# Kernel optimization log

Hardware: AMD Instinct MI355X
Metric: run time of the kernel (lower is better)

The kernel has to match this reference:

```python
import jax, jax.numpy as jnp
import numpy as np

HID = 1024
H = 8
HD = HID // H  # 128; KV length must equal HD for the bias-add broadcast
B = 8
LQ = 4096
LK = HD


def setup_inputs() -> dict:
    key = jax.random.key(0)
    ks = jax.random.split(key, 16)
    s = 0.02
    inp = {
        "query": jax.random.normal(ks[0], (B, LQ, HID), jnp.float32),
        "key": jax.random.normal(ks[1], (B, LK, HID), jnp.float32),
        "value": jax.random.normal(ks[2], (B, LK, HID), jnp.float32),
        "atten": jax.random.normal(ks[3], (B, LQ, HID), jnp.float32),
        "mask": jax.random.randint(ks[4], (B, 1, 1, LK), 0, 2, jnp.int32),
        "Wq": jax.random.normal(ks[5], (HID, HID), jnp.float32) * s,
        "bq": jnp.zeros((HID,), jnp.float32),
        "Wk": jax.random.normal(ks[6], (HID, HID), jnp.float32) * s,
        "bk": jnp.zeros((HID,), jnp.float32),
        "Wv": jax.random.normal(ks[7], (HID, HID), jnp.float32) * s,
        "bv": jnp.zeros((HID,), jnp.float32),
        "Watt": jax.random.normal(ks[8], (HID, HID), jnp.float32) * s,
        "batt": jnp.zeros((HID,), jnp.float32),
        "Wfc": jax.random.normal(ks[9], (HID, HID), jnp.float32) * s,
        "bfc": jnp.zeros((HID,), jnp.float32),
    }
    return inp


def _heads(x):
    # [B, L, HID] -> [B, H, L, HD]
    b, l, _ = x.shape
    return x.reshape(b, l, H, HD).transpose(0, 2, 1, 3)


def reference(query, key, value, atten, mask, Wq, bq, Wk, bk, Wv, bv, Watt, batt, Wfc, bfc):
    scale = jnp.sqrt(jnp.asarray(HD, jnp.float32))
    atten_out = _heads(atten @ Watt.T + batt)          # [B,H,LQ,HD]
    Q = _heads(query @ Wq.T + bq)                      # [B,H,LQ,HD]
    K = _heads(key @ Wk.T + bk)                        # [B,H,LK,HD]
    V = _heads(value @ Wv.T + bv)                      # [B,H,LK,HD]
    energy = jnp.einsum('bhqd,bhkd->bhqk', Q, K) / scale + atten_out  # LK == HD
    energy = jnp.where(mask == 0, jnp.float32(-1e10), energy)
    attention = jax.nn.softmax(energy, axis=-1)
    x = jnp.einsum('bhqk,bhkd->bhqd', attention, V)
    x = x.transpose(0, 2, 1, 3).reshape(query.shape[0], -1, HID)
    return x @ Wfc.T + bfc
```

## Files before the change

### kernel.cpp

```cpp
#include <hip/hip_runtime.h>
#include <hip/hip_bf16.h>
#include <stdint.h>

typedef __bf16 bf16_t;
typedef __bf16 bf16x8 __attribute__((ext_vector_type(8)));
typedef __bf16 bf16x4 __attribute__((ext_vector_type(4)));
typedef float f32x4 __attribute__((ext_vector_type(4)));

#define HIDN 1024
#define NHEAD 8
#define HDIM 128
#define NBATCH 8
#define LQLEN 4096
#define LKLEN 128

__device__ __forceinline__ void gload_lds16(const void* g, void* l) {
  __builtin_amdgcn_global_load_lds(
      (const __attribute__((address_space(1))) unsigned int*)g,
      (__attribute__((address_space(3))) unsigned int*)l, 16, 0, 0);
}

__global__ __launch_bounds__(256) void convk(const float* __restrict__ in,
                                             bf16_t* __restrict__ out, int n4) {
  int i = blockIdx.x * blockDim.x + threadIdx.x;
  const int stride = gridDim.x * blockDim.x;
  for (; i < n4; i += stride) {
    const float4 v = ((const float4*)in)[i];
    bf16x4 o;
    o[0] = (bf16_t)v.x; o[1] = (bf16_t)v.y; o[2] = (bf16_t)v.z; o[3] = (bf16_t)v.w;
    ((bf16x4*)out)[i] = o;
  }
}

template <int MODE>
__global__ __launch_bounds__(512, 2) void gemm8p(const bf16_t* __restrict__ A,
                                                 const bf16_t* __restrict__ Bw,
                                                 const float* __restrict__ bias,
                                                 void* __restrict__ Cout) {
  constexpr int NT = 32;
  constexpr int SLOT = 32768;
  __shared__ uint4 smem_raw[8192];
  char* smem = (char*)smem_raw;

  const int tid = threadIdx.x;
  const int wid = tid >> 6, lane = tid & 63;
  const int lr = lane & 15, lh = lane >> 4;
  const int wr = wid >> 2, wc = wid & 3;

  const int bid = blockIdx.x;
  const int m_blk = (bid & 7) * 16 + (bid >> 5);
  const int n_blk = (bid >> 3) & 3;
  const int m0 = m_blk * 256, n0 = n_blk * 256;

  const int c0 = tid, c1 = tid + 512;
  const int sc0 = (((c0 & 3) ^ ((c0 >> 3) & 3)) << 4);
  const int sc1 = (((c1 & 3) ^ ((c1 >> 3) & 3)) << 4);
  const char* srcA0 = (const char*)A + (size_t)(m0 + (c0 >> 2)) * 2048 + sc0;
  const char* srcA1 = (const char*)A + (size_t)(m0 + (c1 >> 2)) * 2048 + sc1;
  const char* srcB0 = (const char*)Bw + (size_t)(n0 + (c0 >> 2)) * 2048 + sc0;
  const char* srcB1 = (const char*)Bw + (size_t)(n0 + (c1 >> 2)) * 2048 + sc1;
  const int d0 = c0 * 16, d1 = c1 * 16;

  f32x4 acc[8][4] = {};

#pragma unroll
  for (int tt = 0; tt < 3; ++tt) {
    char* dst = smem + tt * SLOT;
    gload_lds16(srcA0 + tt * 64, dst + d0);
    gload_lds16(srcA1 + tt * 64, dst + d1);
    gload_lds16(srcB0 + tt * 64, dst + 16384 + d0);
    gload_lds16(srcB1 + tt * 64, dst + 16384 + d1);
  }
  asm volatile("s_waitcnt vmcnt(8)" ::: "memory");
  __builtin_amdgcn_s_barrier();
  __builtin_amdgcn_sched_barrier(0);

  const int swz = ((lr >> 1) & 3) << 4;
  const int aoff = (wr * 128 + lr) * 64 + ((lh << 4) ^ swz);
  const int boff = 16384 + (wc * 64 + lr) * 64 + ((lh << 4) ^ swz);

  for (int t = 0; t < NT; ++t) {
    const char* sA = smem + (t & 3) * SLOT + aoff;
    const char* sB = smem + (t & 3) * SLOT + boff;
    char* dst = smem + ((t + 3) & 3) * SLOT;
    const int kb = (t + 3) * 64;
    const bool pf = (t <= NT - 4);

    bf16x8 bfr[4], af[8];
#pragma unroll
    for (int n = 0; n < 4; ++n) bfr[n] = *(const bf16x8*)(sB + n * 1024);
#pragma unroll
    for (int m = 0; m < 8; ++m) af[m] = *(const bf16x8*)(sA + m * 1024);
    if (pf) {
      gload_lds16(srcA0 + kb, dst + d0);
      gload_lds16(srcA1 + kb, dst + d1);
      gload_lds16(srcB0 + kb, dst + 16384 + d0);
      gload_lds16(srcB1 + kb, dst + 16384 + d1);
    }
    __builtin_amdgcn_s_setprio(1);
#pragma unroll
    for (int m = 0; m < 8; ++m)
#pragma unroll
      for (int n = 0; n < 4; ++n)
        acc[m][n] = __builtin_amdgcn_mfma_f32_16x16x32_bf16(af[m], bfr[n], acc[m][n], 0, 0, 0);
    __builtin_amdgcn_s_setprio(0);

    if (t < NT - 1) {
      __builtin_amdgcn_sched_barrier(0);
      if (t <= NT - 4)
        asm volatile("s_waitcnt vmcnt(8)" ::: "memory");
      else if (t == NT - 3)
        asm volatile("s_waitcnt vmcnt(4)" ::: "memory");
      else
        asm volatile("s_waitcnt vmcnt(0)" ::: "memory");
      __builtin_amdgcn_s_barrier();
      __builtin_amdgcn_sched_barrier(0);
    }
  }

  if constexpr (MODE == 2) {
    float* C = (float*)Cout;
#pragma unroll
    for (int f = 0; f < 8; ++f) {
      const int gm = m0 + wr * 128 + f * 16 + lh * 4;
#pragma unroll
      for (int j = 0; j < 4; ++j) {
        const int gn = n0 + wc * 64 + j * 16 + lr;
        const float bb = bias[gn];
#pragma unroll
        for (int r = 0; r < 4; ++r)
          C[(size_t)(gm + r) * HIDN + gn] = acc[f][j][r] + bb;
      }
    }
  } else {
    __builtin_amdgcn_s_barrier();
    __builtin_amdgcn_sched_barrier(0);
    char* wlds = smem + wid * 16384;
#pragma unroll
    for (int f = 0; f < 8; ++f) {
#pragma unroll
      for (int j = 0; j < 4; ++j) {
        const int gn = n0 + wc * 64 + j * 16 + lr;
        const float bb = bias[gn];
#pragma unroll
        for (int r = 0; r < 4; ++r)
          *(bf16_t*)(wlds + (f * 16 + lh * 4 + r) * 128 + (j * 16 + lr) * 2) =
              (bf16_t)(acc[f][j][r] + bb);
      }
    }
    asm volatile("s_waitcnt lgkmcnt(0)" ::: "memory");
    __builtin_amdgcn_sched_barrier(0);
    bf16_t* C = (bf16_t*)Cout;
    const int gnb = n0 + wc * 64;
    const int h = gnb >> 7, dd = gnb & 127;
#pragma unroll
    for (int p = 0; p < 16; ++p) {
      const int rl = p * 8 + (lane >> 3);
      const int cb = (lane & 7) * 16;
      const uint4 v = *(const uint4*)(wlds + rl * 128 + cb);
      const int gm = m0 + wr * 128 + rl;
      const int b = gm >> 12, l = gm & 4095;
      char* dstp = (char*)(C + (((size_t)(b * NHEAD + h) * LQLEN + l) << 7) + dd) + cb;
      *(uint4*)dstp = v;
    }
  }
}

template <int MODE, int LROW>
__global__ __launch_bounds__(256) void gemm_bt(const bf16_t* __restrict__ A,
                                               const bf16_t* __restrict__ Bw,
                                               const float* __restrict__ bias,
                                               void* __restrict__ Cout) {
  constexpr int BK = 32;
  __shared__ uint4 AsRaw[128 * BK * 2 / 16];
  __shared__ uint4 BsRaw[128 * BK * 2 / 16];
  bf16_t* As = (bf16_t*)AsRaw;
  bf16_t* Bs = (bf16_t*)BsRaw;

  const int tid = threadIdx.x;
  const int wid = tid >> 6;
  const int lane = tid & 63;
  const int lr = lane & 15, lh = lane >> 4;
  const int m0 = blockIdx.x * 128, n0 = blockIdx.y * 128;
  const int wm = (wid >> 1) * 64, wn = (wid & 1) * 64;

  f32x4 acc[4][4] = {};

  const int srow = lane >> 2;
  const int scol = (lane & 3) * 16;

  for (int k0 = 0; k0 < HIDN; k0 += BK) {
#pragma unroll
    for (int i = 0; i < 2; ++i) {
      const int c = wid + i * 4;
      const int row = c * 16 + srow;
      gload_lds16((const char*)A + ((size_t)(m0 + row) * HIDN + k0) * 2 + scol,
                  (char*)As + c * 1024);
      gload_lds16((const char*)Bw + ((size_t)(n0 + row) * HIDN + k0) * 2 + scol,
                  (char*)Bs + c * 1024);
    }
    __syncthreads();

    bf16x8 af[4], bfr[4];
#pragma unroll
    for (int i = 0; i < 4; ++i) {
      af[i]  = *(const bf16x8*)(As + (wm + i * 16 + lr) * BK + lh * 8);
      bfr[i] = *(const bf16x8*)(Bs + (wn + i * 16 + lr) * BK + lh * 8);
    }
#pragma unroll
    for (int i = 0; i < 4; ++i)
#pragma unroll
      for (int j = 0; j < 4; ++j)
        acc[i][j] = __builtin_amdgcn_mfma_f32_16x16x32_bf16(af[i], bfr[j], acc[i][j], 0, 0, 0);
    __syncthreads();
  }

#pragma unroll
  for (int i = 0; i < 4; ++i) {
#pragma unroll
    for (int r = 0; r < 4; ++r) {
      const int gm = m0 + wm + i * 16 + lh * 4 + r;
#pragma unroll
      for (int j = 0; j < 4; ++j) {
        const int gn = n0 + wn + j * 16 + lr;
        const float v = acc[i][j][r] + bias[gn];
        const int b = gm / LROW, l = gm - b * LROW;
        const int h = gn >> 7, d = gn & 127;
        size_t idx;
        if constexpr (MODE == 0)
          idx = (((size_t)(b * NHEAD + h) * LROW + l) << 7) + d;
        else
          idx = (((size_t)(b * NHEAD + h) * 128 + d) << 7) + l;
        ((bf16_t*)Cout)[idx] = (bf16_t)v;
      }
    }
  }
}

__global__ __launch_bounds__(256) void attn_kernel(
    const bf16_t* __restrict__ Qh, const bf16_t* __restrict__ Ah,
    const bf16_t* __restrict__ Kh, const bf16_t* __restrict__ Vt,
    const int* __restrict__ mask, bf16_t* __restrict__ X) {
  __shared__ uint4 KsRaw[2048];
  __shared__ uint4 VsRaw[2048];
  __shared__ float Ms[128];
  char* Ks = (char*)KsRaw;
  char* Vs = (char*)VsRaw;

  const int tid = threadIdx.x, wid = tid >> 6, lane = tid & 63;
  const int lr = lane & 15, lh = lane >> 4;
  const int bh = blockIdx.y, b = bh >> 3, h = bh & 7;
  const int q0 = blockIdx.x * 64;

  {
    const char* Kg = (const char*)(Kh + (size_t)bh * 16384);
    const char* Vg = (const char*)(Vt + (size_t)bh * 16384);
#pragma unroll
    for (int it = 0; it < 8; ++it) {
      const int e = it * 256 + tid;
      const int row = e >> 4;
      const int cb = (e & 15) << 4;
      const int dst = row * 256 + (cb ^ ((row & 7) << 4));
      *(uint4*)(Ks + dst) = *(const uint4*)(Kg + row * 256 + cb);
      *(uint4*)(Vs + dst) = *(const uint4*)(Vg + row * 256 + cb);
    }
  }
  if (tid < 128) Ms[tid] = (mask[b * 128 + tid] == 0) ? 0.f : 1.f;

  bf16x8 qf[4];
  {
    const bf16_t* Qb = Qh + ((size_t)bh * LQLEN + q0 + wid * 16 + lr) * 128;
#pragma unroll
    for (int s = 0; s < 4; ++s) qf[s] = *(const bf16x8*)(Qb + s * 32 + lh * 8);
  }
  __syncthreads();

  f32x4 acc[8] = {};
#pragma unroll
  for (int nt = 0; nt < 8; ++nt) {
#pragma unroll
    for (int s = 0; s < 4; ++s) {
      const int row = nt * 16 + lr;
      const int cb = (s * 64 + lh * 16) ^ ((row & 7) << 4);
      const bf16x8 kf = *(const bf16x8*)(Ks + row * 256 + cb);
      acc[nt] = __builtin_amdgcn_mfma_f32_16x16x32_bf16(qf[s], kf, acc[nt], 0, 0, 0);
    }
  }

  float ex[8][4];
  float rsum[4];
  const float sc = 0.08838834764831845f;
  const bf16_t* Ab = Ah + ((size_t)bh * LQLEN + q0 + wid * 16) * 128;
#pragma unroll
  for (int r = 0; r < 4; ++r) {
    const int row = lh * 4 + r;
    float mx = -3.0e38f;
#pragma unroll
    for (int nt = 0; nt < 8; ++nt) {
      const int col = nt * 16 + lr;
      float e = acc[nt][r] * sc + (float)Ab[row * 128 + col];
      e = (Ms[col] != 0.f) ? e : -1.0e10f;
      ex[nt][r] = e;
      mx = fmaxf(mx, e);
    }
    mx = fmaxf(mx, __shfl_xor(mx, 1));
    mx = fmaxf(mx, __shfl_xor(mx, 2));
    mx = fmaxf(mx, __shfl_xor(mx, 4));
    mx = fmaxf(mx, __shfl_xor(mx, 8));
    float s_ = 0.f;
#pragma unroll
    for (int nt = 0; nt < 8; ++nt) {
      const float p = expf(ex[nt][r] - mx);
      ex[nt][r] = p;
      s_ += p;
    }
    s_ += __shfl_xor(s_, 1);
    s_ += __shfl_xor(s_, 2);
    s_ += __shfl_xor(s_, 4);
    s_ += __shfl_xor(s_, 8);
    rsum[r] = s_;
  }

  __syncthreads();
  char* Pb = Ks + wid * 4096;
#pragma unroll
  for (int r = 0; r < 4; ++r) {
    const int row = lh * 4 + r;
#pragma unroll
    for (int nt = 0; nt < 8; ++nt) {
      const int col = nt * 16 + lr;
      const int off = (row * 256 + col * 2) ^ ((row & 7) << 4);
      *(bf16_t*)(Pb + off) = (bf16_t)ex[nt][r];
    }
  }
  __syncthreads();

  bf16x8 pf[4];
#pragma unroll
  for (int s = 0; s < 4; ++s)
    pf[s] = *(const bf16x8*)(Pb + lr * 256 + ((s * 64 + lh * 16) ^ ((lr & 7) << 4)));
  f32x4 acc2[8] = {};
#pragma unroll
  for (int nt = 0; nt < 8; ++nt) {
#pragma unroll
    for (int s = 0; s < 4; ++s) {
      const int row = nt * 16 + lr;
      const int cb = (s * 64 + lh * 16) ^ ((row & 7) << 4);
      const bf16x8 vf = *(const bf16x8*)(Vs + row * 256 + cb);
      acc2[nt] = __builtin_amdgcn_mfma_f32_16x16x32_bf16(pf[s], vf, acc2[nt], 0, 0, 0);
    }
  }

  float rs[4];
#pragma unroll
  for (int r = 0; r < 4; ++r) rs[r] = 1.f / rsum[r];
  bf16_t* Xb = X + ((size_t)b * LQLEN + q0 + wid * 16) * HIDN + h * 128;
#pragma unroll
  for (int nt = 0; nt < 8; ++nt)
#pragma unroll
    for (int r = 0; r < 4; ++r)
      Xb[(size_t)(lh * 4 + r) * HIDN + nt * 16 + lr] = (bf16_t)(acc2[nt][r] * rs[r]);
}

extern "C" void kernel_launch(void* const* d_in, const int* in_sizes, int n_in,
                              void* d_out, int out_size, void* d_ws, size_t ws_size,
                              hipStream_t stream) {
  const float* query = (const float*)d_in[0];
  const float* key   = (const float*)d_in[1];
  const float* value = (const float*)d_in[2];
  const float* atten = (const float*)d_in[3];
  const int*   mask  = (const int*)d_in[4];
  const float* Wq  = (const float*)d_in[5];  const float* bq   = (const float*)d_in[6];
  const float* Wk  = (const float*)d_in[7];  const float* bk   = (const float*)d_in[8];
  const float* Wv  = (const float*)d_in[9];  const float* bv   = (const float*)d_in[10];
  const float* Wat = (const float*)d_in[11]; const float* batt = (const float*)d_in[12];
  const float* Wfc = (const float*)d_in[13]; const float* bfc  = (const float*)d_in[14];

  char* ws = (char*)d_ws;
  bf16_t* qbf = (bf16_t*)(ws + 0x0000000);
  bf16_t* abf = (bf16_t*)(ws + 0x4000000);
  bf16_t* Qh  = (bf16_t*)(ws + 0x8000000);
  bf16_t* Ah  = (bf16_t*)(ws + 0xC000000);
  char* sm = ws + 0x10000000;
  bf16_t* kbf = (bf16_t*)(sm + 0x000000);
  bf16_t* vbf = (bf16_t*)(sm + 0x200000);
  bf16_t* wqb = (bf16_t*)(sm + 0x400000);
  bf16_t* wkb = (bf16_t*)(sm + 0x600000);
  bf16_t* wvb = (bf16_t*)(sm + 0x800000);
  bf16_t* wab = (bf16_t*)(sm + 0xA00000);
  bf16_t* wfb = (bf16_t*)(sm + 0xC00000);
  bf16_t* Kh  = (bf16_t*)(sm + 0xE00000);
  bf16_t* Vt  = (bf16_t*)(sm + 0x1000000);
  bf16_t* X   = qbf;

  auto conv = [&](const float* src, bf16_t* dst, int n) {
    const int n4 = n >> 2;
    int g = (n4 + 255) >> 8; if (g > 2048) g = 2048;
    convk<<<dim3(g), dim3(256), 0, stream>>>(src, dst, n4);
  };
  conv(query, qbf, NBATCH * LQLEN * HIDN);
  conv(atten, abf, NBATCH * LQLEN * HIDN);
  conv(key,   kbf, NBATCH * LKLEN * HIDN);
  conv(value, vbf, NBATCH * LKLEN * HIDN);
  conv(Wq,  wqb, HIDN * HIDN);
  conv(Wk,  wkb, HIDN * HIDN);
  conv(Wv,  wvb, HIDN * HIDN);
  conv(Wat, wab, HIDN * HIDN);
  conv(Wfc, wfb, HIDN * HIDN);

  gemm_bt<0, 128><<<dim3(8, 8), dim3(256), 0, stream>>>(kbf, wkb, bk, (void*)Kh);
  gemm_bt<1, 128><<<dim3(8, 8), dim3(256), 0, stream>>>(vbf, wvb, bv, (void*)Vt);

  gemm8p<0><<<dim3(512), dim3(512), 0, stream>>>(qbf, wqb, bq, (void*)Qh);
  gemm8p<0><<<dim3(512), dim3(512), 0, stream>>>(abf, wab, batt, (void*)Ah);

  attn_kernel<<<dim3(LQLEN / 64, NBATCH * NHEAD), dim3(256), 0, stream>>>(
      Qh, Ah, Kh, Vt, mask, X);

  gemm8p<2><<<dim3(512), dim3(512), 0, stream>>>(X, wfb, bfc, d_out);
}
```

Measured before the change: 466.8 us.

## Fuse fp32-to-bf16 conversion of activations into GEMM loads; batch weight conversions

The Q and attention projection GEMMs now read fp32 activations directly through registers, convert them to bf16 and write them to LDS inside a software-pipelined loop. This removes the separate full-size conversion passes over query and atten. The seven small conversions are merged into one launch. The attention kernel also stages the Ah tile in LDS with async loads and writes its output through LDS as coalesced 16-byte stores. In exchange, the A path now uses register staging rather than direct-to-LDS loads, which raises register pressure and makes the waitcnt bookkeeping more delicate.

```diff
diff --git a/kernel.cpp b/kernel.cpp
--- a/kernel.cpp
+++ b/kernel.cpp
@@ -4,7 +4,6 @@
 
 typedef __bf16 bf16_t;
 typedef __bf16 bf16x8 __attribute__((ext_vector_type(8)));
-typedef __bf16 bf16x4 __attribute__((ext_vector_type(4)));
 typedef float f32x4 __attribute__((ext_vector_type(4)));
 
 #define HIDN 1024
@@ -20,20 +19,33 @@
       (__attribute__((address_space(3))) unsigned int*)l, 16, 0, 0);
 }
 
-__global__ __launch_bounds__(256) void convk(const float* __restrict__ in,
-                                             bf16_t* __restrict__ out, int n4) {
-  int i = blockIdx.x * blockDim.x + threadIdx.x;
-  const int stride = gridDim.x * blockDim.x;
-  for (; i < n4; i += stride) {
-    const float4 v = ((const float4*)in)[i];
-    bf16x4 o;
+__global__ __launch_bounds__(256) void convk7(
+    const float* s0, const float* s1, const float* s2, const float* s3,
+    const float* s4, const float* s5, const float* s6,
+    bf16_t* d0, bf16_t* d1, bf16_t* d2, bf16_t* d3,
+    bf16_t* d4, bf16_t* d5, bf16_t* d6) {
+  const float* src; bf16_t* dst;
+  switch (blockIdx.y) {
+    case 0: src = s0; dst = d0; break;
+    case 1: src = s1; dst = d1; break;
+    case 2: src = s2; dst = d2; break;
+    case 3: src = s3; dst = d3; break;
+    case 4: src = s4; dst = d4; break;
+    case 5: src = s5; dst = d5; break;
+    default: src = s6; dst = d6; break;
+  }
+  const int n4 = (1024 * 1024) / 4;
+  const int stride = gridDim.x * 256;
+  for (int i = blockIdx.x * 256 + threadIdx.x; i < n4; i += stride) {
+    const float4 v = ((const float4*)src)[i];
+    bf16x8 o;
     o[0] = (bf16_t)v.x; o[1] = (bf16_t)v.y; o[2] = (bf16_t)v.z; o[3] = (bf16_t)v.w;
-    ((bf16x4*)out)[i] = o;
+    *(uint2*)((char*)dst + (size_t)i * 8) = *(uint2*)&o;
   }
 }
 
-template <int MODE>
-__global__ __launch_bounds__(512, 2) void gemm8p(const bf16_t* __restrict__ A,
+template <int MODE, bool AF32>
+__global__ __launch_bounds__(512, 2) void gemm8p(const void* __restrict__ Asrc,
                                                  const bf16_t* __restrict__ Bw,
                                                  const float* __restrict__ bias,
                                                  void* __restrict__ Cout) {
@@ -53,70 +65,162 @@
   const int m0 = m_blk * 256, n0 = n_blk * 256;
 
   const int c0 = tid, c1 = tid + 512;
-  const int sc0 = (((c0 & 3) ^ ((c0 >> 3) & 3)) << 4);
-  const int sc1 = (((c1 & 3) ^ ((c1 >> 3) & 3)) << 4);
-  const char* srcA0 = (const char*)A + (size_t)(m0 + (c0 >> 2)) * 2048 + sc0;
-  const char* srcA1 = (const char*)A + (size_t)(m0 + (c1 >> 2)) * 2048 + sc1;
-  const char* srcB0 = (const char*)Bw + (size_t)(n0 + (c0 >> 2)) * 2048 + sc0;
-  const char* srcB1 = (const char*)Bw + (size_t)(n0 + (c1 >> 2)) * 2048 + sc1;
+  const int sl0 = ((c0 & 3) ^ ((c0 >> 3) & 3));
+  const int sl1 = ((c1 & 3) ^ ((c1 >> 3) & 3));
+  const char* srcB0 = (const char*)Bw + (size_t)(n0 + (c0 >> 2)) * 2048 + (sl0 << 4);
+  const char* srcB1 = (const char*)Bw + (size_t)(n0 + (c1 >> 2)) * 2048 + (sl1 << 4);
   const int d0 = c0 * 16, d1 = c1 * 16;
 
   f32x4 acc[8][4] = {};
-
-#pragma unroll
-  for (int tt = 0; tt < 3; ++tt) {
-    char* dst = smem + tt * SLOT;
-    gload_lds16(srcA0 + tt * 64, dst + d0);
-    gload_lds16(srcA1 + tt * 64, dst + d1);
-    gload_lds16(srcB0 + tt * 64, dst + 16384 + d0);
-    gload_lds16(srcB1 + tt * 64, dst + 16384 + d1);
-  }
-  asm volatile("s_waitcnt vmcnt(8)" ::: "memory");
-  __builtin_amdgcn_s_barrier();
-  __builtin_amdgcn_sched_barrier(0);
 
   const int swz = ((lr >> 1) & 3) << 4;
   const int aoff = (wr * 128 + lr) * 64 + ((lh << 4) ^ swz);
   const int boff = 16384 + (wc * 64 + lr) * 64 + ((lh << 4) ^ swz);
 
-  for (int t = 0; t < NT; ++t) {
-    const char* sA = smem + (t & 3) * SLOT + aoff;
-    const char* sB = smem + (t & 3) * SLOT + boff;
-    char* dst = smem + ((t + 3) & 3) * SLOT;
-    const int kb = (t + 3) * 64;
-    const bool pf = (t <= NT - 4);
-
-    bf16x8 bfr[4], af[8];
-#pragma unroll
-    for (int n = 0; n < 4; ++n) bfr[n] = *(const bf16x8*)(sB + n * 1024);
-#pragma unroll
-    for (int m = 0; m < 8; ++m) af[m] = *(const bf16x8*)(sA + m * 1024);
-    if (pf) {
-      gload_lds16(srcA0 + kb, dst + d0);
-      gload_lds16(srcA1 + kb, dst + d1);
-      gload_lds16(srcB0 + kb, dst + 16384 + d0);
-      gload_lds16(srcB1 + kb, dst + 16384 + d1);
-    }
-    __builtin_amdgcn_s_setprio(1);
-#pragma unroll
-    for (int m = 0; m < 8; ++m)
-#pragma unroll
-      for (int n = 0; n < 4; ++n)
-        acc[m][n] = __builtin_amdgcn_mfma_f32_16x16x32_bf16(af[m], bfr[n], acc[m][n], 0, 0, 0);
-    __builtin_amdgcn_s_setprio(0);
-
-    if (t < NT - 1) {
-      __builtin_amdgcn_sched_barrier(0);
-      if (t <= NT - 4)
-        asm volatile("s_waitcnt vmcnt(8)" ::: "memory");
-      else if (t == NT - 3)
-        asm volatile("s_waitcnt vmcnt(4)" ::: "memory");
-      else
-        asm volatile("s_waitcnt vmcnt(0)" ::: "memory");
-      __builtin_amdgcn_s_barrier();
-      __builtin_amdgcn_sched_barrier(0);
-    }
-  }
+#define GLOADB(T)                                                     \
+  do {                                                                \
+    char* bdst = smem + (((T) & 3) * SLOT) + 16384;                   \
+    gload_lds16(srcB0 + (T) * 64, bdst + d0);                         \
+    gload_lds16(srcB1 + (T) * 64, bdst + d1);                         \
+  } while (0)
+
+  if constexpr (AF32) {
+    const char* srcAf0 = (const char*)Asrc + (size_t)(m0 + (c0 >> 2)) * 4096 + sl0 * 32;
+    const char* srcAf1 = (const char*)Asrc + (size_t)(m0 + (c1 >> 2)) * 4096 + sl1 * 32;
+
+    f32x4 eA0, eA1, eA2, eA3, oA0, oA1, oA2, oA3;
+
+#define ISSUE_A(R0, R1, R2, R3, T)                                    \
+  do {                                                                \
+    R0 = *(const f32x4*)(srcAf0 + (T) * 128);                         \
+    R1 = *(const f32x4*)(srcAf0 + (T) * 128 + 16);                    \
+    R2 = *(const f32x4*)(srcAf1 + (T) * 128);                         \
+    R3 = *(const f32x4*)(srcAf1 + (T) * 128 + 16);                    \
+  } while (0)
+
+#define WRITE_A(SL, R0, R1, R2, R3)                                   \
+  do {                                                                \
+    bf16x8 w0, w1;                                                    \
+    w0[0] = (bf16_t)R0[0]; w0[1] = (bf16_t)R0[1];                     \
+    w0[2] = (bf16_t)R0[2]; w0[3] = (bf16_t)R0[3];                     \
+    w0[4] = (bf16_t)R1[0]; w0[5] = (bf16_t)R1[1];                     \
+    w0[6] = (bf16_t)R1[2]; w0[7] = (bf16_t)R1[3];                     \
+    w1[0] = (bf16_t)R2[0]; w1[1] = (bf16_t)R2[1];                     \
+    w1[2] = (bf16_t)R2[2]; w1[3] = (bf16_t)R2[3];                     \
+    w1[4] = (bf16_t)R3[0]; w1[5] = (bf16_t)R3[1];                     \
+    w1[6] = (bf16_t)R3[2]; w1[7] = (bf16_t)R3[3];                     \
+    *(bf16x8*)(smem + (SL) * SLOT + d0) = w0;                         \
+    *(bf16x8*)(smem + (SL) * SLOT + d1) = w1;                         \
+  } while (0)
+
+    ISSUE_A(eA0, eA1, eA2, eA3, 0);
+    ISSUE_A(oA0, oA1, oA2, oA3, 1);
+    asm volatile("" ::: "memory");
+    GLOADB(0); GLOADB(1); GLOADB(2);
+    asm volatile("" ::: "memory");
+    asm volatile("s_waitcnt vmcnt(6)" ::: "memory");
+    WRITE_A(0, eA0, eA1, eA2, eA3);
+    WRITE_A(1, oA0, oA1, oA2, oA3);
+    ISSUE_A(eA0, eA1, eA2, eA3, 2);
+    ISSUE_A(oA0, oA1, oA2, oA3, 3);
+    asm volatile("" ::: "memory");
+    asm volatile("s_waitcnt vmcnt(4) lgkmcnt(0)" ::: "memory");
+    __builtin_amdgcn_s_barrier();
+    __builtin_amdgcn_sched_barrier(0);
+
+#define GTILE(T, R0, R1, R2, R3)                                          \
+  do {                                                                    \
+    const char* sA = smem + ((T) & 3) * SLOT + aoff;                      \
+    const char* sB = smem + ((T) & 3) * SLOT + boff;                      \
+    if ((T) <= NT - 3) WRITE_A(((T) + 2) & 3, R0, R1, R2, R3);            \
+    if ((T) <= NT - 5) ISSUE_A(R0, R1, R2, R3, (T) + 4);                  \
+    if ((T) <= NT - 4) GLOADB((T) + 3);                                   \
+    bf16x8 bfr[4], af[8];                                                 \
+    _Pragma("unroll") for (int n = 0; n < 4; ++n)                         \
+        bfr[n] = *(const bf16x8*)(sB + n * 1024);                         \
+    _Pragma("unroll") for (int m = 0; m < 8; ++m)                         \
+        af[m] = *(const bf16x8*)(sA + m * 1024);                          \
+    __builtin_amdgcn_s_setprio(1);                                        \
+    _Pragma("unroll") for (int m = 0; m < 8; ++m)                         \
+        _Pragma("unroll") for (int n = 0; n < 4; ++n)                     \
+            acc[m][n] = __builtin_amdgcn_mfma_f32_16x16x32_bf16(          \
+                af[m], bfr[n], acc[m][n], 0, 0, 0);                       \
+    __builtin_amdgcn_s_setprio(0);                                        \
+    if ((T) < NT - 1) {                                                   \
+      __builtin_amdgcn_sched_barrier(0);                                  \
+      if ((T) <= NT - 5)                                                  \
+        asm volatile("s_waitcnt vmcnt(6) lgkmcnt(0)" ::: "memory");       \
+      else if ((T) <= NT - 3)                                             \
+        asm volatile("s_waitcnt vmcnt(2) lgkmcnt(0)" ::: "memory");       \
+      else                                                                \
+        asm volatile("s_waitcnt vmcnt(0) lgkmcnt(0)" ::: "memory");       \
+      __builtin_amdgcn_s_barrier();                                       \
+      __builtin_amdgcn_sched_barrier(0);                                  \
+    }                                                                     \
+  } while (0)
+
+    for (int tt = 0; tt < NT / 2; ++tt) {
+      GTILE(2 * tt, eA0, eA1, eA2, eA3);
+      GTILE(2 * tt + 1, oA0, oA1, oA2, oA3);
+    }
+#undef GTILE
+#undef ISSUE_A
+#undef WRITE_A
+  } else {
+    const char* srcA0 = (const char*)Asrc + (size_t)(m0 + (c0 >> 2)) * 2048 + (sl0 << 4);
+    const char* srcA1 = (const char*)Asrc + (size_t)(m0 + (c1 >> 2)) * 2048 + (sl1 << 4);
+#pragma unroll
+    for (int tt = 0; tt < 3; ++tt) {
+      char* dst = smem + tt * SLOT;
+      gload_lds16(srcA0 + tt * 64, dst + d0);
+      gload_lds16(srcA1 + tt * 64, dst + d1);
+      gload_lds16(srcB0 + tt * 64, dst + 16384 + d0);
+      gload_lds16(srcB1 + tt * 64, dst + 16384 + d1);
+    }
+    asm volatile("s_waitcnt vmcnt(8)" ::: "memory");
+    __builtin_amdgcn_s_barrier();
+    __builtin_amdgcn_sched_barrier(0);
+
+    for (int t = 0; t < NT; ++t) {
+      const char* sA = smem + (t & 3) * SLOT + aoff;
+      const char* sB = smem + (t & 3) * SLOT + boff;
+      char* dst = smem + ((t + 3) & 3) * SLOT;
+      const int kb = (t + 3) * 64;
+      const bool pf = (t <= NT - 4);
+
+      bf16x8 bfr[4], af[8];
+#pragma unroll
+      for (int n = 0; n < 4; ++n) bfr[n] = *(const bf16x8*)(sB + n * 1024);
+#pragma unroll
+      for (int m = 0; m < 8; ++m) af[m] = *(const bf16x8*)(sA + m * 1024);
+      if (pf) {
+        gload_lds16(srcA0 + kb, dst + d0);
+        gload_lds16(srcA1 + kb, dst + d1);
+        gload_lds16(srcB0 + kb, dst + 16384 + d0);
+        gload_lds16(srcB1 + kb, dst + 16384 + d1);
+      }
+      __builtin_amdgcn_s_setprio(1);
+#pragma unroll
+      for (int m = 0; m < 8; ++m)
+#pragma unroll
+        for (int n = 0; n < 4; ++n)
+          acc[m][n] = __builtin_amdgcn_mfma_f32_16x16x32_bf16(af[m], bfr[n], acc[m][n], 0, 0, 0);
+      __builtin_amdgcn_s_setprio(0);
+
+      if (t < NT - 1) {
+        __builtin_amdgcn_sched_barrier(0);
+        if (t <= NT - 4)
+          asm volatile("s_waitcnt vmcnt(8)" ::: "memory");
+        else if (t == NT - 3)
+          asm volatile("s_waitcnt vmcnt(4)" ::: "memory");
+        else
+          asm volatile("s_waitcnt vmcnt(0)" ::: "memory");
+        __builtin_amdgcn_s_barrier();
+        __builtin_amdgcn_sched_barrier(0);
+      }
+    }
+  }
+#undef GLOADB
 
   if constexpr (MODE == 2) {
     float* C = (float*)Cout;
@@ -286,19 +390,32 @@
       acc[nt] = __builtin_amdgcn_mfma_f32_16x16x32_bf16(qf[s], kf, acc[nt], 0, 0, 0);
     }
   }
+  __syncthreads();
+
+  {
+    const char* Ag = (const char*)(Ah + ((size_t)bh * LQLEN + q0) * 128);
+#pragma unroll
+    for (int it = 0; it < 4; ++it) {
+      const int c = it * 256 + tid;
+      gload_lds16(Ag + c * 16, Ks + 16384 + c * 16);
+    }
+  }
+  asm volatile("s_waitcnt vmcnt(0)" ::: "memory");
+  __syncthreads();
+  const char* Al = Ks + 16384;
 
   float ex[8][4];
   float rsum[4];
   const float sc = 0.08838834764831845f;
-  const bf16_t* Ab = Ah + ((size_t)bh * LQLEN + q0 + wid * 16) * 128;
 #pragma unroll
   for (int r = 0; r < 4; ++r) {
     const int row = lh * 4 + r;
+    const int rowg = wid * 16 + row;
     float mx = -3.0e38f;
 #pragma unroll
     for (int nt = 0; nt < 8; ++nt) {
       const int col = nt * 16 + lr;
-      float e = acc[nt][r] * sc + (float)Ab[row * 128 + col];
+      float e = acc[nt][r] * sc + (float)(*(const bf16_t*)(Al + rowg * 256 + col * 2));
       e = (Ms[col] != 0.f) ? e : -1.0e10f;
       ex[nt][r] = e;
       mx = fmaxf(mx, e);
@@ -321,7 +438,6 @@
     rsum[r] = s_;
   }
 
-  __syncthreads();
   char* Pb = Ks + wid * 4096;
 #pragma unroll
   for (int r = 0; r < 4; ++r) {
@@ -350,16 +466,29 @@
       acc2[nt] = __builtin_amdgcn_mfma_f32_16x16x32_bf16(pf[s], vf, acc2[nt], 0, 0, 0);
     }
   }
+  __syncthreads();
 
   float rs[4];
 #pragma unroll
   for (int r = 0; r < 4; ++r) rs[r] = 1.f / rsum[r];
-  bf16_t* Xb = X + ((size_t)b * LQLEN + q0 + wid * 16) * HIDN + h * 128;
 #pragma unroll
   for (int nt = 0; nt < 8; ++nt)
 #pragma unroll
     for (int r = 0; r < 4; ++r)
-      Xb[(size_t)(lh * 4 + r) * HIDN + nt * 16 + lr] = (bf16_t)(acc2[nt][r] * rs[r]);
+      *(bf16_t*)(Vs + (wid * 16 + lh * 4 + r) * 256 + (nt * 16 + lr) * 2) =
+          (bf16_t)(acc2[nt][r] * rs[r]);
+  asm volatile("s_waitcnt lgkmcnt(0)" ::: "memory");
+  __syncthreads();
+
+#pragma unroll
+  for (int it = 0; it < 4; ++it) {
+    const int c = it * 256 + tid;
+    const int row = c >> 4;
+    const int off = (c & 15) << 4;
+    const uint4 v = *(const uint4*)(Vs + row * 256 + off);
+    char* dstp = (char*)(X + ((size_t)(b * LQLEN) + q0 + row) * HIDN + h * 128) + off;
+    *(uint4*)dstp = v;
+  }
 }
 
 extern "C" void kernel_launch(void* const* d_in, const int* in_sizes, int n_in,
@@ -377,8 +506,7 @@
   const float* Wfc = (const float*)d_in[13]; const float* bfc  = (const float*)d_in[14];
 
   char* ws = (char*)d_ws;
-  bf16_t* qbf = (bf16_t*)(ws + 0x0000000);
-  bf16_t* abf = (bf16_t*)(ws + 0x4000000);
+  bf16_t* X   = (bf16_t*)(ws + 0x0000000);
   bf16_t* Qh  = (bf16_t*)(ws + 0x8000000);
   bf16_t* Ah  = (bf16_t*)(ws + 0xC000000);
   char* sm = ws + 0x10000000;
@@ -391,31 +519,19 @@
   bf16_t* wfb = (bf16_t*)(sm + 0xC00000);
   bf16_t* Kh  = (bf16_t*)(sm + 0xE00000);
   bf16_t* Vt  = (bf16_t*)(sm + 0x1000000);
-  bf16_t* X   = qbf;
-
-  auto conv = [&](const float* src, bf16_t* dst, int n) {
-    const int n4 = n >> 2;
-    int g = (n4 + 255) >> 8; if (g > 2048) g = 2048;
-    convk<<<dim3(g), dim3(256), 0, stream>>>(src, dst, n4);
-  };
-  conv(query, qbf, NBATCH * LQLEN * HIDN);
-  conv(atten, abf, NBATCH * LQLEN * HIDN);
-  conv(key,   kbf, NBATCH * LKLEN * HIDN);
-  conv(value, vbf, NBATCH * LKLEN * HIDN);
-  conv(Wq,  wqb, HIDN * HIDN);
-  conv(Wk,  wkb, HIDN * HIDN);
-  conv(Wv,  wvb, HIDN * HIDN);
-  conv(Wat, wab, HIDN * HIDN);
-  conv(Wfc, wfb, HIDN * HIDN);
+
+  convk7<<<dim3(256, 7), dim3(256), 0, stream>>>(
+      key, value, Wq, Wk, Wv, Wat, Wfc,
+      kbf, vbf, wqb, wkb, wvb, wab, wfb);
 
   gemm_bt<0, 128><<<dim3(8, 8), dim3(256), 0, stream>>>(kbf, wkb, bk, (void*)Kh);
   gemm_bt<1, 128><<<dim3(8, 8), dim3(256), 0, stream>>>(vbf, wvb, bv, (void*)Vt);
 
-  gemm8p<0><<<dim3(512), dim3(512), 0, stream>>>(qbf, wqb, bq, (void*)Qh);
-  gemm8p<0><<<dim3(512), dim3(512), 0, stream>>>(abf, wab, batt, (void*)Ah);
+  gemm8p<0, true><<<dim3(512), dim3(512), 0, stream>>>(query, wqb, bq, (void*)Qh);
+  gemm8p<0, true><<<dim3(512), dim3(512), 0, stream>>>(atten, wab, batt, (void*)Ah);
 
   attn_kernel<<<dim3(LQLEN / 64, NBATCH * NHEAD), dim3(256), 0, stream>>>(
       Qh, Ah, Kh, Vt, mask, X);
 
-  gemm8p<2><<<dim3(512), dim3(512), 0, stream>>>(X, wfb, bfc, d_out);
+  gemm8p<2, false><<<dim3(512), dim3(512), 0, stream>>>(X, wfb, bfc, d_out);
 }
```

Measured after the change: 413.2 us. 11.5% less time.
